# Kernel tuning notes

Hardware: AMD Instinct MI355X
Metric: run time of the kernel (lower is better)

Reference implementation:

```python
import jax, jax.numpy as jnp
import numpy as np

N = 14541   # num entities (FB15k-237)
R = 64      # num relations / edge types
E = 16384   # edges per relation
F = 128     # feature_dim
H = 128     # hidden_dim
O = 64      # out_dim
LH = O // 2 # lstm hidden per direction


def setup_inputs() -> dict:
    key = jax.random.key(0)
    ks = jax.random.split(key, 12)
    s = 0.05
    return {
        "node_ids": jnp.arange(N, dtype=jnp.int32),
        "src": jax.random.randint(ks[0], (R, E), 0, N, dtype=jnp.int32),
        "dst": jax.random.randint(ks[1], (R, E), 0, N, dtype=jnp.int32),
        "entity_emb": jax.random.normal(ks[2], (N, F), jnp.float32) * s,
        "W1": jax.random.normal(ks[3], (R, F, H), jnp.float32) * s,
        "b1": jax.random.normal(ks[4], (R, H), jnp.float32) * s,
        "W2": jax.random.normal(ks[5], (R, H, O), jnp.float32) * s,
        "b2": jax.random.normal(ks[6], (R, O), jnp.float32) * s,
        "w_ih": jax.random.normal(ks[7], (2, 4 * LH, O), jnp.float32) * s,
        "w_hh": jax.random.normal(ks[8], (2, 4 * LH, LH), jnp.float32) * s,
        "b_ih": jax.random.normal(ks[9], (2, 4 * LH), jnp.float32) * s,
        "b_hh": jax.random.normal(ks[10], (2, 4 * LH), jnp.float32) * s,
    }


def hetero_graph_conv(x, src, dst, W, b):
    """DGL HeteroGraphConv({rel: GraphConv(norm='both')}, aggregate='mean').
    x: [N, Fin]; src/dst: [R, E]; W: [R, Fin, Fout]; b: [R, Fout]."""
    n = x.shape[0]
    rid = jnp.arange(R, dtype=src.dtype)[:, None]
    fsrc = (rid * n + src).reshape(-1)            # per-(relation,node) flat ids
    fdst = (rid * n + dst).reshape(-1)
    ones = jnp.ones(fsrc.shape[0], x.dtype)
    deg_out = jax.ops.segment_sum(ones, fsrc, R * n)  # [R*N]
    deg_in = jax.ops.segment_sum(ones, fdst, R * n)
    norm_out = jnp.where(deg_out > 0, deg_out, 1.0) ** -0.5
    norm_in = jnp.where(deg_in > 0, deg_in, 1.0) ** -0.5
    # gather-normalize-scatter (sum) per relation, norm='both'
    msg = x[src.reshape(-1)] * norm_out[fsrc][:, None]     # [R*E, Fin]
    agg = jax.ops.segment_sum(msg, fdst, R * n)            # [R*N, Fin]
    agg = (agg * norm_in[:, None]).reshape(R, n, -1)
    out = jnp.einsum('rnf,rfo->rno', agg, W) + b[:, None, :]
    return out.mean(axis=0)  # mean aggregate across relations -> [N, Fout]


def lstm_one_step(x, w_ih, b_ih, b_hh):
    """Single-timestep LSTM direction with zero initial (h, c). PyTorch gate order i,f,g,o."""
    gates = x @ w_ih.T + b_ih + b_hh              # [N, 4*LH]
    i, f, g, o = jnp.split(gates, 4, axis=-1)
    c = jax.nn.sigmoid(i) * jnp.tanh(g)           # f*c0 = 0
    return jax.nn.sigmoid(o) * jnp.tanh(c)


def reference(node_ids, src, dst, entity_emb, W1, b1, W2, b2, w_ih, w_hh, b_ih, b_hh):
    x = entity_emb[node_ids]                                   # embedding lookup [N, F]
    h = jax.nn.relu(hetero_graph_conv(x, src, dst, W1, b1))    # conv1 + ReLU
    h = hetero_graph_conv(h, src, dst, W2, b2)                 # conv2 -> [N, O]
    # BiLSTM over seq_len=1 (unsqueeze(1) in torch): h0=c0=0 so W_hh contributes nothing
    h_fwd = lstm_one_step(h, w_ih[0], b_ih[0], b_hh[0])
    h_bwd = lstm_one_step(h, w_ih[1], b_ih[1], b_hh[1])
    return jnp.concatenate([h_fwd, h_bwd], axis=-1)            # [N, O]
```

## Files before the change

### kernel.cpp

```cpp
#include <hip/hip_runtime.h>

#define NN 14541
#define RR 64
#define EE 16384
#define EMAX (RR * EE)
#define RN (RR * NN)
#define NT 64
#define TILES 228
#define RGROUPS 8
#define RPG 8
#define NBPT 58
#define NWORDS (NBPT * 256 / 2)

typedef unsigned short u16;
typedef __attribute__((ext_vector_type(8))) short bf16x8;
typedef __attribute__((ext_vector_type(4))) float f32x4;

__device__ __forceinline__ u16 f2b(float f) {
  unsigned u = __builtin_bit_cast(unsigned, f);
  u += 0x7fffu + ((u >> 16) & 1u);
  return (u16)(u >> 16);
}
__device__ __forceinline__ float b2f(short h) {
  unsigned u = ((unsigned)(u16)h) << 16;
  return __builtin_bit_cast(float, u);
}
__device__ __forceinline__ unsigned cvtpk(float lo, float hi) {
  unsigned r;
  asm("v_cvt_pk_bf16_f32 %0, %1, %2" : "=v"(r) : "v"(lo), "v"(hi));
  return r;
}
__device__ __forceinline__ float sigm(float x) { return 1.0f / (1.0f + expf(-x)); }

__device__ __forceinline__ void gload_lds16(const void* g, void* l) {
  __builtin_amdgcn_global_load_lds(
      (const __attribute__((address_space(1))) unsigned int*)g,
      (__attribute__((address_space(3))) unsigned int*)l, 16, 0, 0);
}

__global__ __launch_bounds__(256) void build_k(
    const int* __restrict__ src, const int* __restrict__ dst,
    int* __restrict__ row_ptr, int* __restrict__ ssrc,
    float* __restrict__ scoef, float* __restrict__ tmpc,
    const float* __restrict__ W1, const float* __restrict__ W2,
    const float* __restrict__ b1, const float* __restrict__ b2,
    const float* __restrict__ emb,
    u16* __restrict__ W1T, u16* __restrict__ W2T,
    u16* __restrict__ emb_bf, float* __restrict__ mb1, float* __restrict__ mb2)
{
  __shared__ __align__(16) unsigned smem[NWORDS * 2];
  __shared__ int wsum[4];
  const int b = blockIdx.x, t = threadIdx.x;

  if (b < 64) {
    unsigned* cd = smem;
    unsigned* cs = smem + NWORDS;
    const int r = b;
    const int ebase = r * EE;

    for (int i = t; i < NWORDS; i += 256) { cd[i] = 0; cs[i] = 0; }
    __syncthreads();
    for (int e = t; e < EE; e += 256) {
      int d = dst[ebase + e], s = src[ebase + e];
      atomicAdd(&cd[d >> 1], (d & 1) ? 0x10000u : 1u);
      atomicAdd(&cs[s >> 1], (s & 1) ? 0x10000u : 1u);
    }
    __syncthreads();
    for (int e = t; e < EE; e += 256) {
      int d = dst[ebase + e], s = src[ebase + e];
      int cdd = (cd[d >> 1] >> ((d & 1) * 16)) & 0xffff;
      int css = (cs[s >> 1] >> ((s & 1) * 16)) & 0xffff;
      tmpc[ebase + e] = rsqrtf((float)cdd) * rsqrtf((float)css) * 0.015625f;
    }
    const int base = t * (NBPT / 2);
    int tot = 0;
    #pragma unroll
    for (int j = 0; j < NBPT / 2; j++) {
      unsigned w = cd[base + j];
      tot += (int)(w & 0xffff) + (int)(w >> 16);
    }
    const int lane = t & 63, wv = t >> 6;
    int x = tot;
    #pragma unroll
    for (int o = 1; o < 64; o <<= 1) { int y = __shfl_up(x, o, 64); if (lane >= o) x += y; }
    if (lane == 63) wsum[wv] = x;
    __syncthreads();
    int runl = x - tot;
    #pragma unroll
    for (int j = 0; j < 3; j++) if (j < wv) runl += wsum[j];
    const int nb0 = t * NBPT;
    #pragma unroll
    for (int j = 0; j < NBPT / 2; j++) {
      unsigned w = cd[base + j];
      int c0 = (int)(w & 0xffff), c1 = (int)(w >> 16);
      int n0 = nb0 + 2 * j;
      if (n0 <= NN)     row_ptr[r * NN + n0]     = r * EE + runl;
      if (n0 + 1 <= NN) row_ptr[r * NN + n0 + 1] = r * EE + runl + c0;
      cd[base + j] = (unsigned)(runl | ((runl + c0) << 16));
      runl += c0 + c1;
    }
    __syncthreads();
    for (int e = t; e < EE; e += 256) {
      int d = dst[ebase + e], s = src[ebase + e];
      unsigned old = atomicAdd(&cd[d >> 1], (d & 1) ? 0x10000u : 1u);
      int slot = ebase + (int)((old >> ((d & 1) * 16)) & 0xffff);
      ssrc[slot] = s;
      scoef[slot] = tmpc[ebase + e];
    }
    return;
  }

  float (*T)[65] = (float(*)[65])smem;
  const int bb = b - 64;
  if (bb < 128) {
    const int h = t & 63, kof = t >> 6;
    const int r = bb >> 1, hbase = (bb & 1) << 6;
    const float* Wr = W1 + (r << 14) + hbase;
    for (int k0 = 0; k0 < 128; k0 += 4) {
      int k = k0 + kof;
      T[k][h] = Wr[k * 128 + h];
    }
    __syncthreads();
    u16* dstp = W1T + (r << 14) + hbase * 128;
    #pragma unroll
    for (int it = 0; it < 4; ++it) {
      int p = it * 256 + t;
      int hh = p >> 4, v = p & 15;
      int hg = hbase + hh;
      bf16x8 o;
      #pragma unroll
      for (int j = 0; j < 8; j++)
        o[j] = (short)f2b(T[((v ^ (hg & 7)) << 3) + j][hh]);
      *(bf16x8*)(dstp + hh * 128 + v * 8) = o;
    }
  } else if (bb < 192) {
    const int h = t & 63, kof = t >> 6;
    const int r = bb - 128;
    const float* Wr = W2 + (r << 13);
    for (int k0 = 0; k0 < 128; k0 += 4) {
      int k = k0 + kof;
      T[k][h] = Wr[k * 64 + h];
    }
    __syncthreads();
    u16* dstp = W2T + (r << 13);
    #pragma unroll
    for (int it = 0; it < 4; ++it) {
      int p = it * 256 + t;
      int hh = p >> 4, v = p & 15;
      bf16x8 o;
      #pragma unroll
      for (int j = 0; j < 8; j++)
        o[j] = (short)f2b(T[((v ^ (hh & 7)) << 3) + j][hh]);
      *(bf16x8*)(dstp + hh * 128 + v * 8) = o;
    }
  } else if (bb < 2011) {
    int i = ((bb - 192) * 256 + t) * 4;
    if (i < NN * 128) {
      float4 vv = *(const float4*)(emb + i);
      ushort4 o;
      o.x = f2b(vv.x); o.y = f2b(vv.y); o.z = f2b(vv.z); o.w = f2b(vv.w);
      *(ushort4*)(emb_bf + i) = o;
    }
  } else {
    if (t < 128) { float s = 0.f; for (int r = 0; r < RR; r++) s += b1[r * 128 + t]; mb1[t] = s * (1.f/64.f); }
    if (t < 64)  { float s = 0.f; for (int r = 0; r < RR; r++) s += b2[r * 64 + t];  mb2[t] = s * (1.f/64.f); }
  }
}

__global__ __launch_bounds__(256, 2) void conv1_k(
    const u16* __restrict__ emb_bf, const int* __restrict__ row_ptr,
    const int* __restrict__ ssrc, const float* __restrict__ scoef,
    const u16* __restrict__ W1T, float* __restrict__ out1, int gstr)
{
  __shared__ __align__(16) u16 Bs[128 * 128];

  const int tid = threadIdx.x;
  const int g = blockIdx.x & 7, t = blockIdx.x >> 3;
  const int nb = t * NT;
  const int lane = tid & 63, wid = tid >> 6, c15 = lane & 15, kg = lane >> 4;
  const int rq = lane >> 2, q = lane & 3;
  const int nq = nb + wid * 16 + rq;
  const int srcl = c15 * 4 + kg;
  const int gbase = g * RPG;

  f32x4 acc[8];
  #pragma unroll
  for (int b = 0; b < 8; b++) acc[b] = (f32x4){0.f, 0.f, 0.f, 0.f};

  int rc0 = row_ptr[gbase * NN + nq];
  int rc1 = row_ptr[gbase * NN + nq + 1];
  int ps[4]; float pc[4];
  {
    const int d0 = rc1 - rc0;
    #pragma unroll
    for (int m = 0; m < 4; m++) {
      ps[m] = 0; pc[m] = 0.f;
      if (m < d0) { ps[m] = ssrc[rc0 + m]; pc[m] = scoef[rc0 + m]; }
    }
  }

  for (int rr = 0; rr < RPG; ++rr) {
    const int r = gbase + rr;
    {
      const u16* src_g = W1T + (r << 14);
      #pragma unroll
      for (int it = 0; it < 8; ++it)
        gload_lds16(src_g + (it * 256 + tid) * 8, (u16*)Bs + (it * 256 + wid * 64) * 8);
    }
    int nr0 = 0, nr1 = 0;
    if (rr + 1 < RPG) { nr0 = row_ptr[(r + 1) * NN + nq]; nr1 = row_ptr[(r + 1) * NN + nq + 1]; }
    const int d = rc1 - rc0;
    float a[4][8];
    #pragma unroll
    for (int w = 0; w < 4; w++)
      #pragma unroll
      for (int j = 0; j < 8; j++) a[w][j] = 0.f;
    #pragma unroll
    for (int m = 0; m < 4; m++) {
      if (m < d) {
        const bf16x8* xr = (const bf16x8*)(emb_bf + (size_t)ps[m] * 128);
        #pragma unroll
        for (int w = 0; w < 4; w++) {
          bf16x8 v = xr[w * 4 + q];
          #pragma unroll
          for (int j = 0; j < 8; j++) a[w][j] = fmaf(pc[m], b2f(v[j]), a[w][j]);
        }
      }
    }
    for (int p = 4; __any(p < d); ++p) {
      if (p < d) {
        int sx = ssrc[rc0 + p];
        float c = scoef[rc0 + p];
        const bf16x8* xr = (const bf16x8*)(emb_bf + (size_t)sx * 128);
        #pragma unroll
        for (int w = 0; w < 4; w++) {
          bf16x8 v = xr[w * 4 + q];
          #pragma unroll
          for (int j = 0; j < 8; j++) a[w][j] = fmaf(c, b2f(v[j]), a[w][j]);
        }
      }
    }
    int qs[4]; float qc[4];
    {
      const int ndg = nr1 - nr0;
      #pragma unroll
      for (int m = 0; m < 4; m++) {
        qs[m] = 0; qc[m] = 0.f;
        if (m < ndg) { qs[m] = ssrc[nr0 + m]; qc[m] = scoef[nr0 + m]; }
      }
    }
    bf16x8 af[4];
    #pragma unroll
    for (int kk = 0; kk < 4; kk++) {
      unsigned w0 = cvtpk(a[kk][0], a[kk][1]);
      unsigned w1 = cvtpk(a[kk][2], a[kk][3]);
      unsigned w2 = cvtpk(a[kk][4], a[kk][5]);
      unsigned w3 = cvtpk(a[kk][6], a[kk][7]);
      uint4 uu;
      uu.x = (unsigned)__shfl((int)w0, srcl);
      uu.y = (unsigned)__shfl((int)w1, srcl);
      uu.z = (unsigned)__shfl((int)w2, srcl);
      uu.w = (unsigned)__shfl((int)w3, srcl);
      af[kk] = __builtin_bit_cast(bf16x8, uu);
    }
    __syncthreads();
    #pragma unroll
    for (int tc = 0; tc < 8; tc++) {
      const int hh = tc * 16 + c15;
      #pragma unroll
      for (int kk = 0; kk < 4; kk++) {
        int u = kk * 4 + kg;
        bf16x8 bfr = *(const bf16x8*)(Bs + hh * 128 + ((u ^ (hh & 7)) << 3));
        acc[tc] = __builtin_amdgcn_mfma_f32_16x16x32_bf16(af[kk], bfr, acc[tc], 0, 0, 0);
      }
    }
    rc0 = nr0; rc1 = nr1;
    #pragma unroll
    for (int m = 0; m < 4; m++) { ps[m] = qs[m]; pc[m] = qc[m]; }
    if (rr + 1 < RPG) __syncthreads();
  }
  float* base = out1 + (size_t)g * gstr;
  #pragma unroll
  for (int qi = 0; qi < 4; qi++) {
    const int nn2 = nb + wid * 16 + kg * 4 + qi;
    if (nn2 < NN) {
      float* po = base + (size_t)nn2 * 128 + c15;
      if (gstr) {
        #pragma unroll
        for (int tc = 0; tc < 8; tc++) po[tc * 16] = acc[tc][qi];
      } else {
        #pragma unroll
        for (int tc = 0; tc < 8; tc++) atomicAdd(po + tc * 16, acc[tc][qi]);
      }
    }
  }
}

__global__ void relu_k(const float* __restrict__ out1, const float* __restrict__ mb1,
                       u16* __restrict__ h1, int gstr) {
  int i = (blockIdx.x * 256 + threadIdx.x) * 4;
  if (i >= NN * 128) return;
  f32x4 v = *(const f32x4*)(mb1 + (i & 127));
  if (gstr) {
    #pragma unroll
    for (int g = 0; g < RGROUPS; g++)
      v += __builtin_nontemporal_load((const f32x4*)(out1 + (size_t)g * gstr + i));
  } else {
    v += *(const f32x4*)(out1 + i);
  }
  ushort4 o;
  o.x = f2b(v.x > 0.f ? v.x : 0.f);
  o.y = f2b(v.y > 0.f ? v.y : 0.f);
  o.z = f2b(v.z > 0.f ? v.z : 0.f);
  o.w = f2b(v.w > 0.f ? v.w : 0.f);
  *(ushort4*)(h1 + i) = o;
}

__global__ __launch_bounds__(256, 2) void conv2_k(
    const u16* __restrict__ h1, const int* __restrict__ row_ptr,
    const int* __restrict__ ssrc, const float* __restrict__ scoef,
    const u16* __restrict__ W2T, float* __restrict__ out2, int gstr)
{
  __shared__ __align__(16) u16 Bs[2][64 * 128];

  const int tid = threadIdx.x;
  const int g = blockIdx.x & 7, t = blockIdx.x >> 3;
  const int nb = t * NT;
  const int lane = tid & 63, wid = tid >> 6, c15 = lane & 15, kg = lane >> 4;
  const int rq = lane >> 2, q = lane & 3;
  const int nq = nb + wid * 16 + rq;
  const int srcl = c15 * 4 + kg;
  const int gbase = g * RPG;

  f32x4 acc[4];
  #pragma unroll
  for (int b = 0; b < 4; b++) acc[b] = (f32x4){0.f, 0.f, 0.f, 0.f};

  int rc0 = row_ptr[gbase * NN + nq];
  int rc1 = row_ptr[gbase * NN + nq + 1];
  int ps[4]; float pc[4];
  {
    const int d0 = rc1 - rc0;
    #pragma unroll
    for (int m = 0; m < 4; m++) {
      ps[m] = 0; pc[m] = 0.f;
      if (m < d0) { ps[m] = ssrc[rc0 + m]; pc[m] = scoef[rc0 + m]; }
    }
  }
  {
    const u16* src_g = W2T + (gbase << 13);
    #pragma unroll
    for (int it = 0; it < 4; ++it)
      gload_lds16(src_g + (it * 256 + tid) * 8, (u16*)Bs[0] + (it * 256 + wid * 64) * 8);
  }

  for (int rr = 0; rr < RPG; ++rr) {
    const int r = gbase + rr;
    if (rr + 1 < RPG) {
      const u16* src_g = W2T + ((r + 1) << 13);
      #pragma unroll
      for (int it = 0; it < 4; ++it)
        gload_lds16(src_g + (it * 256 + tid) * 8, (u16*)Bs[(rr + 1) & 1] + (it * 256 + wid * 64) * 8);
    }
    int nr0 = 0, nr1 = 0;
    if (rr + 1 < RPG) { nr0 = row_ptr[(r + 1) * NN + nq]; nr1 = row_ptr[(r + 1) * NN + nq + 1]; }
    const int d = rc1 - rc0;
    float a[4][8];
    #pragma unroll
    for (int w = 0; w < 4; w++)
      #pragma unroll
      for (int j = 0; j < 8; j++) a[w][j] = 0.f;
    #pragma unroll
    for (int m = 0; m < 4; m++) {
      if (m < d) {
        const bf16x8* xr = (const bf16x8*)(h1 + (size_t)ps[m] * 128);
        #pragma unroll
        for (int w = 0; w < 4; w++) {
          bf16x8 v = xr[w * 4 + q];
          #pragma unroll
          for (int j = 0; j < 8; j++) a[w][j] = fmaf(pc[m], b2f(v[j]), a[w][j]);
        }
      }
    }
    for (int p = 4; __any(p < d); ++p) {
      if (p < d) {
        int sx = ssrc[rc0 + p];
        float c = scoef[rc0 + p];
        const bf16x8* xr = (const bf16x8*)(h1 + (size_t)sx * 128);
        #pragma unroll
        for (int w = 0; w < 4; w++) {
          bf16x8 v = xr[w * 4 + q];
          #pragma unroll
          for (int j = 0; j < 8; j++) a[w][j] = fmaf(c, b2f(v[j]), a[w][j]);
        }
      }
    }
    int qs[4]; float qc[4];
    {
      const int ndg = nr1 - nr0;
      #pragma unroll
      for (int m = 0; m < 4; m++) {
        qs[m] = 0; qc[m] = 0.f;
        if (m < ndg) { qs[m] = ssrc[nr0 + m]; qc[m] = scoef[nr0 + m]; }
      }
    }
    bf16x8 af[4];
    #pragma unroll
    for (int kk = 0; kk < 4; kk++) {
      unsigned w0 = cvtpk(a[kk][0], a[kk][1]);
      unsigned w1 = cvtpk(a[kk][2], a[kk][3]);
      unsigned w2 = cvtpk(a[kk][4], a[kk][5]);
      unsigned w3 = cvtpk(a[kk][6], a[kk][7]);
      uint4 uu;
      uu.x = (unsigned)__shfl((int)w0, srcl);
      uu.y = (unsigned)__shfl((int)w1, srcl);
      uu.z = (unsigned)__shfl((int)w2, srcl);
      uu.w = (unsigned)__shfl((int)w3, srcl);
      af[kk] = __builtin_bit_cast(bf16x8, uu);
    }
    __syncthreads();
    const u16* Bcur = Bs[rr & 1];
    #pragma unroll
    for (int tc = 0; tc < 4; tc++) {
      const int hh = tc * 16 + c15;
      #pragma unroll
      for (int kk = 0; kk < 4; kk++) {
        int u = kk * 4 + kg;
        bf16x8 bfr = *(const bf16x8*)(Bcur + hh * 128 + ((u ^ (hh & 7)) << 3));
        acc[tc] = __builtin_amdgcn_mfma_f32_16x16x32_bf16(af[kk], bfr, acc[tc], 0, 0, 0);
      }
    }
    rc0 = nr0; rc1 = nr1;
    #pragma unroll
    for (int m = 0; m < 4; m++) { ps[m] = qs[m]; pc[m] = qc[m]; }
  }
  float* base = out2 + (size_t)g * gstr;
  #pragma unroll
  for (int qi = 0; qi < 4; qi++) {
    const int nn2 = nb + wid * 16 + kg * 4 + qi;
    if (nn2 < NN) {
      float* po = base + (size_t)nn2 * 64 + c15;
      if (gstr) {
        #pragma unroll
        for (int tc = 0; tc < 4; tc++) po[tc * 16] = acc[tc][qi];
      } else {
        #pragma unroll
        for (int tc = 0; tc < 4; tc++) atomicAdd(po + tc * 16, acc[tc][qi]);
      }
    }
  }
}

__global__ __launch_bounds__(256) void lstm_k(const float* __restrict__ out2, const float* __restrict__ mb2,
                                              const float* __restrict__ w_ih, const float* __restrict__ b_ih,
                                              const float* __restrict__ b_hh, float* __restrict__ out,
                                              int gstr) {
  __shared__ float hs[16][64];
  const int tid = threadIdx.x, s = tid >> 6, k = tid & 63;
  const int nb = blockIdx.x * 16;
  #pragma unroll
  for (int j = 0; j < 4; j++) {
    int n = nb + s * 4 + j;
    if (n < NN) {
      float v = mb2[k];
      if (gstr) {
        #pragma unroll
        for (int g = 0; g < RGROUPS; g++)
          v += __builtin_nontemporal_load(out2 + (size_t)g * gstr + n * 64 + k);
      } else {
        v += out2[n * 64 + k];
      }
      hs[s * 4 + j][k] = v;
    }
  }
  __syncthreads();
  const int d = k >> 5, jj = k & 31;
  const float* wb = w_ih + d * 128 * 64;
  const float bi = b_ih[d * 128 + jj]      + b_hh[d * 128 + jj];
  const float bg = b_ih[d * 128 + 64 + jj] + b_hh[d * 128 + 64 + jj];
  const float bo = b_ih[d * 128 + 96 + jj] + b_hh[d * 128 + 96 + jj];
  const float* wi = wb + jj * 64;
  const float* wg = wb + (64 + jj) * 64;
  const float* wo = wb + (96 + jj) * 64;
  float gi[4] = {bi, bi, bi, bi}, gg[4] = {bg, bg, bg, bg}, go[4] = {bo, bo, bo, bo};
  #pragma unroll 8
  for (int kk = 0; kk < 64; kk++) {
    float w_i = wi[kk], w_g = wg[kk], w_o = wo[kk];
    #pragma unroll
    for (int j = 0; j < 4; j++) {
      float hv = hs[s * 4 + j][kk];
      gi[j] = fmaf(hv, w_i, gi[j]);
      gg[j] = fmaf(hv, w_g, gg[j]);
      go[j] = fmaf(hv, w_o, go[j]);
    }
  }
  #pragma unroll
  for (int j = 0; j < 4; j++) {
    int n = nb + s * 4 + j;
    if (n < NN) {
      float c = sigm(gi[j]) * tanhf(gg[j]);
      out[n * 64 + k] = sigm(go[j]) * tanhf(c);
    }
  }
}

extern "C" void kernel_launch(void* const* d_in, const int* in_sizes, int n_in,
                              void* d_out, int out_size, void* d_ws, size_t ws_size,
                              hipStream_t stream) {
  const int*   src  = (const int*)d_in[1];
  const int*   dst  = (const int*)d_in[2];
  const float* emb  = (const float*)d_in[3];
  const float* W1   = (const float*)d_in[4];
  const float* b1   = (const float*)d_in[5];
  const float* W2   = (const float*)d_in[6];
  const float* b2   = (const float*)d_in[7];
  const float* w_ih = (const float*)d_in[8];
  const float* b_ih = (const float*)d_in[10];
  const float* b_hh = (const float*)d_in[11];
  float* out = (float*)d_out;

  char* ws = (char*)d_ws;
  size_t off = 0;
  float* out1f  = (float*)(ws + off); off += (size_t)NN * 128 * 4;
  float* out2f  = (float*)(ws + off); off += (size_t)NN * 64 * 4;
  size_t zb_fb = off;
  int*   row_ptr= (int*)(ws + off);   off += (size_t)(RN + 256) * 4;
  int*   ssrc   = (int*)(ws + off);   off += (size_t)EMAX * 4;
  float* scoef  = (float*)(ws + off); off += (size_t)EMAX * 4;
  float* tmpc   = (float*)(ws + off); off += (size_t)EMAX * 4;
  u16*   emb_bf = (u16*)(ws + off);   off += (size_t)NN * 128 * 2;
  u16*   h1     = (u16*)(ws + off);   off += (size_t)NN * 128 * 2;
  u16*   W1T    = (u16*)(ws + off);   off += (size_t)RR * 128 * 128 * 2;
  u16*   W2T    = (u16*)(ws + off);   off += (size_t)RR * 64 * 128 * 2;
  float* mb1    = (float*)(ws + off); off += 512;
  float* mb2    = (float*)(ws + off); off += 256;
  float* out1g  = (float*)(ws + off); off += (size_t)RGROUPS * NN * 128 * 4;
  float* out2g  = (float*)(ws + off); off += (size_t)RGROUPS * NN * 64 * 4;

  const bool slices = ws_size >= off;
  float* o1 = slices ? out1g : out1f;
  float* o2 = slices ? out2g : out2f;
  const int gs1 = slices ? NN * 128 : 0;
  const int gs2 = slices ? NN * 64 : 0;

  if (!slices) hipMemsetAsync(d_ws, 0, zb_fb, stream);
  build_k<<<64 + 2012, 256, 0, stream>>>(src, dst, row_ptr, ssrc, scoef, tmpc,
                                         W1, W2, b1, b2, emb, W1T, W2T, emb_bf, mb1, mb2);
  conv1_k<<<TILES * RGROUPS, 256, 0, stream>>>(emb_bf, row_ptr, ssrc, scoef, W1T, o1, gs1);
  relu_k<<<(NN * 128 / 4 + 255) / 256, 256, 0, stream>>>(o1, mb1, h1, gs1);
  conv2_k<<<TILES * RGROUPS, 256, 0, stream>>>(h1, row_ptr, ssrc, scoef, W2T, o2, gs2);
  lstm_k<<<(NN + 15) / 16, 256, 0, stream>>>(o2, mb2, w_ih, b_ih, b_hh, out, gs2);
}
```

Baseline: 311.8 us.

## Fuse ReLU and LSTM epilogues into conv kernels via last-block counters

Removes the separate relu_k and lstm_k launches. Each conv kernel now bumps a per-tile atomic counter after writing its relation-group partial. The last of the 8 group blocks for that tile sums the slices and applies bias+ReLU (conv1) or the bias plus the LSTM gate math (conv2). This saves two launches and lets the reduction read partials that may still be in cache. In exchange it adds threadfence/atomic synchronisation and a serial tail done by only one block per tile, and the counters are reset in build_k.

After: 529.8 us. 69.9% more time.

```diff
diff --git a/kernel.cpp b/kernel.cpp
--- a/kernel.cpp
+++ b/kernel.cpp
@@ -46,7 +46,8 @@
     const float* __restrict__ b1, const float* __restrict__ b2,
     const float* __restrict__ emb,
     u16* __restrict__ W1T, u16* __restrict__ W2T,
-    u16* __restrict__ emb_bf, float* __restrict__ mb1, float* __restrict__ mb2)
+    u16* __restrict__ emb_bf, float* __restrict__ mb1, float* __restrict__ mb2,
+    int* __restrict__ cnt)
 {
   __shared__ __align__(16) unsigned smem[NWORDS * 2];
   __shared__ int wsum[4];
@@ -164,15 +165,18 @@
   } else {
     if (t < 128) { float s = 0.f; for (int r = 0; r < RR; r++) s += b1[r * 128 + t]; mb1[t] = s * (1.f/64.f); }
     if (t < 64)  { float s = 0.f; for (int r = 0; r < RR; r++) s += b2[r * 64 + t];  mb2[t] = s * (1.f/64.f); }
+    for (int i = t; i < 512; i += 256) cnt[i] = 0;
   }
 }
 
 __global__ __launch_bounds__(256, 2) void conv1_k(
     const u16* __restrict__ emb_bf, const int* __restrict__ row_ptr,
     const int* __restrict__ ssrc, const float* __restrict__ scoef,
-    const u16* __restrict__ W1T, float* __restrict__ out1, int gstr)
+    const u16* __restrict__ W1T, float* __restrict__ out1, int gstr,
+    const float* __restrict__ mb1, u16* __restrict__ h1, int* __restrict__ cnt1)
 {
   __shared__ __align__(16) u16 Bs[128 * 128];
+  __shared__ int lastf;
 
   const int tid = threadIdx.x;
   const int g = blockIdx.x & 7, t = blockIdx.x >> 3;
@@ -279,49 +283,68 @@
     for (int m = 0; m < 4; m++) { ps[m] = qs[m]; pc[m] = qc[m]; }
     if (rr + 1 < RPG) __syncthreads();
   }
-  float* base = out1 + (size_t)g * gstr;
-  #pragma unroll
-  for (int qi = 0; qi < 4; qi++) {
-    const int nn2 = nb + wid * 16 + kg * 4 + qi;
-    if (nn2 < NN) {
-      float* po = base + (size_t)nn2 * 128 + c15;
-      if (gstr) {
-        #pragma unroll
-        for (int tc = 0; tc < 8; tc++) po[tc * 16] = acc[tc][qi];
-      } else {
-        #pragma unroll
-        for (int tc = 0; tc < 8; tc++) atomicAdd(po + tc * 16, acc[tc][qi]);
-      }
-    }
-  }
-}
-
-__global__ void relu_k(const float* __restrict__ out1, const float* __restrict__ mb1,
-                       u16* __restrict__ h1, int gstr) {
-  int i = (blockIdx.x * 256 + threadIdx.x) * 4;
-  if (i >= NN * 128) return;
-  f32x4 v = *(const f32x4*)(mb1 + (i & 127));
-  if (gstr) {
-    #pragma unroll
-    for (int g = 0; g < RGROUPS; g++)
-      v += __builtin_nontemporal_load((const f32x4*)(out1 + (size_t)g * gstr + i));
-  } else {
-    v += *(const f32x4*)(out1 + i);
-  }
-  ushort4 o;
-  o.x = f2b(v.x > 0.f ? v.x : 0.f);
-  o.y = f2b(v.y > 0.f ? v.y : 0.f);
-  o.z = f2b(v.z > 0.f ? v.z : 0.f);
-  o.w = f2b(v.w > 0.f ? v.w : 0.f);
-  *(ushort4*)(h1 + i) = o;
+  {
+    float* base = out1 + (size_t)g * gstr;
+    #pragma unroll
+    for (int qi = 0; qi < 4; qi++) {
+      const int nn2 = nb + wid * 16 + kg * 4 + qi;
+      if (nn2 < NN) {
+        float* po = base + (size_t)nn2 * 128 + c15;
+        if (gstr) {
+          #pragma unroll
+          for (int tc = 0; tc < 8; tc++) po[tc * 16] = acc[tc][qi];
+        } else {
+          #pragma unroll
+          for (int tc = 0; tc < 8; tc++) atomicAdd(po + tc * 16, acc[tc][qi]);
+        }
+      }
+    }
+  }
+  __syncthreads();
+  if (tid == 0) {
+    __threadfence();
+    int old = atomicAdd(&cnt1[t], 1);
+    lastf = (old == RGROUPS - 1) ? 1 : 0;
+    if (lastf) __threadfence();
+  }
+  __syncthreads();
+  if (lastf) {
+    #pragma unroll
+    for (int it = 0; it < 8; ++it) {
+      int idx = it * 256 + tid;
+      int row = idx >> 5, col4 = (idx & 31) * 4;
+      int n = nb + row;
+      if (n < NN) {
+        size_t o = (size_t)n * 128 + col4;
+        f32x4 v = *(const f32x4*)(mb1 + col4);
+        if (gstr) {
+          #pragma unroll
+          for (int g2 = 0; g2 < RGROUPS; g2++)
+            v += *(const f32x4*)(out1 + (size_t)g2 * gstr + o);
+        } else {
+          v += *(const f32x4*)(out1 + o);
+        }
+        ushort4 ov;
+        ov.x = f2b(v.x > 0.f ? v.x : 0.f);
+        ov.y = f2b(v.y > 0.f ? v.y : 0.f);
+        ov.z = f2b(v.z > 0.f ? v.z : 0.f);
+        ov.w = f2b(v.w > 0.f ? v.w : 0.f);
+        *(ushort4*)(h1 + o) = ov;
+      }
+    }
+  }
 }
 
 __global__ __launch_bounds__(256, 2) void conv2_k(
     const u16* __restrict__ h1, const int* __restrict__ row_ptr,
     const int* __restrict__ ssrc, const float* __restrict__ scoef,
-    const u16* __restrict__ W2T, float* __restrict__ out2, int gstr)
+    const u16* __restrict__ W2T, float* __restrict__ out2, int gstr,
+    const float* __restrict__ mb2, const float* __restrict__ w_ih,
+    const float* __restrict__ b_ih, const float* __restrict__ b_hh,
+    float* __restrict__ outF, int* __restrict__ cnt2)
 {
   __shared__ __align__(16) u16 Bs[2][64 * 128];
+  __shared__ int lastf;
 
   const int tid = threadIdx.x;
   const int g = blockIdx.x & 7, t = blockIdx.x >> 3;
@@ -434,72 +457,82 @@
     #pragma unroll
     for (int m = 0; m < 4; m++) { ps[m] = qs[m]; pc[m] = qc[m]; }
   }
-  float* base = out2 + (size_t)g * gstr;
+  {
+    float* base = out2 + (size_t)g * gstr;
+    #pragma unroll
+    for (int qi = 0; qi < 4; qi++) {
+      const int nn2 = nb + wid * 16 + kg * 4 + qi;
+      if (nn2 < NN) {
+        float* po = base + (size_t)nn2 * 64 + c15;
+        if (gstr) {
+          #pragma unroll
+          for (int tc = 0; tc < 4; tc++) po[tc * 16] = acc[tc][qi];
+        } else {
+          #pragma unroll
+          for (int tc = 0; tc < 4; tc++) atomicAdd(po + tc * 16, acc[tc][qi]);
+        }
+      }
+    }
+  }
+  __syncthreads();
+  if (tid == 0) {
+    __threadfence();
+    int old = atomicAdd(&cnt2[t], 1);
+    lastf = (old == RGROUPS - 1) ? 1 : 0;
+    if (lastf) __threadfence();
+  }
+  __syncthreads();
+  if (!lastf) return;
+
+  float* hs = (float*)Bs;
   #pragma unroll
-  for (int qi = 0; qi < 4; qi++) {
-    const int nn2 = nb + wid * 16 + kg * 4 + qi;
-    if (nn2 < NN) {
-      float* po = base + (size_t)nn2 * 64 + c15;
+  for (int it = 0; it < 16; ++it) {
+    int idx = it * 256 + tid;
+    int row = idx >> 6, k = idx & 63;
+    int n = nb + row;
+    float v = mb2[k];
+    if (n < NN) {
       if (gstr) {
         #pragma unroll
-        for (int tc = 0; tc < 4; tc++) po[tc * 16] = acc[tc][qi];
+        for (int g2 = 0; g2 < RGROUPS; g2++)
+          v += out2[(size_t)g2 * gstr + (size_t)n * 64 + k];
       } else {
-        #pragma unroll
-        for (int tc = 0; tc < 4; tc++) atomicAdd(po + tc * 16, acc[tc][qi]);
-      }
-    }
-  }
-}
-
-__global__ __launch_bounds__(256) void lstm_k(const float* __restrict__ out2, const float* __restrict__ mb2,
-                                              const float* __restrict__ w_ih, const float* __restrict__ b_ih,
-                                              const float* __restrict__ b_hh, float* __restrict__ out,
-                                              int gstr) {
-  __shared__ float hs[16][64];
-  const int tid = threadIdx.x, s = tid >> 6, k = tid & 63;
-  const int nb = blockIdx.x * 16;
-  #pragma unroll
-  for (int j = 0; j < 4; j++) {
-    int n = nb + s * 4 + j;
-    if (n < NN) {
-      float v = mb2[k];
-      if (gstr) {
-        #pragma unroll
-        for (int g = 0; g < RGROUPS; g++)
-          v += __builtin_nontemporal_load(out2 + (size_t)g * gstr + n * 64 + k);
-      } else {
-        v += out2[n * 64 + k];
-      }
-      hs[s * 4 + j][k] = v;
-    }
+        v += out2[(size_t)n * 64 + k];
+      }
+    }
+    hs[row * 64 + k] = v;
   }
   __syncthreads();
-  const int d = k >> 5, jj = k & 31;
-  const float* wb = w_ih + d * 128 * 64;
-  const float bi = b_ih[d * 128 + jj]      + b_hh[d * 128 + jj];
-  const float bg = b_ih[d * 128 + 64 + jj] + b_hh[d * 128 + 64 + jj];
-  const float bo = b_ih[d * 128 + 96 + jj] + b_hh[d * 128 + 96 + jj];
+  const int k = tid & 63, sg = tid >> 6;
+  const int dd = k >> 5, jj = k & 31;
+  const float* wb = w_ih + dd * 128 * 64;
+  const float bi = b_ih[dd * 128 + jj]      + b_hh[dd * 128 + jj];
+  const float bg = b_ih[dd * 128 + 64 + jj] + b_hh[dd * 128 + 64 + jj];
+  const float bo = b_ih[dd * 128 + 96 + jj] + b_hh[dd * 128 + 96 + jj];
   const float* wi = wb + jj * 64;
   const float* wg = wb + (64 + jj) * 64;
   const float* wo = wb + (96 + jj) * 64;
-  float gi[4] = {bi, bi, bi, bi}, gg[4] = {bg, bg, bg, bg}, go[4] = {bo, bo, bo, bo};
-  #pragma unroll 8
+  float gi[16], gg[16], go[16];
+  #pragma unroll
+  for (int j = 0; j < 16; j++) { gi[j] = bi; gg[j] = bg; go[j] = bo; }
+  #pragma unroll 4
   for (int kk = 0; kk < 64; kk++) {
     float w_i = wi[kk], w_g = wg[kk], w_o = wo[kk];
-    #pragma unroll
-    for (int j = 0; j < 4; j++) {
-      float hv = hs[s * 4 + j][kk];
+    const float* hrow = hs + (sg * 16) * 64 + kk;
+    #pragma unroll
+    for (int j = 0; j < 16; j++) {
+      float hv = hrow[j * 64];
       gi[j] = fmaf(hv, w_i, gi[j]);
       gg[j] = fmaf(hv, w_g, gg[j]);
       go[j] = fmaf(hv, w_o, go[j]);
     }
   }
   #pragma unroll
-  for (int j = 0; j < 4; j++) {
-    int n = nb + s * 4 + j;
+  for (int j = 0; j < 16; j++) {
+    int n = nb + sg * 16 + j;
     if (n < NN) {
       float c = sigm(gi[j]) * tanhf(gg[j]);
-      out[n * 64 + k] = sigm(go[j]) * tanhf(c);
+      outF[(size_t)n * 64 + k] = sigm(go[j]) * tanhf(c);
     }
   }
 }
@@ -534,6 +567,7 @@
   u16*   W2T    = (u16*)(ws + off);   off += (size_t)RR * 64 * 128 * 2;
   float* mb1    = (float*)(ws + off); off += 512;
   float* mb2    = (float*)(ws + off); off += 256;
+  int*   cnt    = (int*)(ws + off);   off += 512 * 4;
   float* out1g  = (float*)(ws + off); off += (size_t)RGROUPS * NN * 128 * 4;
   float* out2g  = (float*)(ws + off); off += (size_t)RGROUPS * NN * 64 * 4;
 
@@ -545,9 +579,9 @@
 
   if (!slices) hipMemsetAsync(d_ws, 0, zb_fb, stream);
   build_k<<<64 + 2012, 256, 0, stream>>>(src, dst, row_ptr, ssrc, scoef, tmpc,
-                                         W1, W2, b1, b2, emb, W1T, W2T, emb_bf, mb1, mb2);
-  conv1_k<<<TILES * RGROUPS, 256, 0, stream>>>(emb_bf, row_ptr, ssrc, scoef, W1T, o1, gs1);
-  relu_k<<<(NN * 128 / 4 + 255) / 256, 256, 0, stream>>>(o1, mb1, h1, gs1);
-  conv2_k<<<TILES * RGROUPS, 256, 0, stream>>>(h1, row_ptr, ssrc, scoef, W2T, o2, gs2);
-  lstm_k<<<(NN + 15) / 16, 256, 0, stream>>>(o2, mb2, w_ih, b_ih, b_hh, out, gs2);
-}
+                                         W1, W2, b1, b2, emb, W1T, W2T, emb_bf, mb1, mb2, cnt);
+  conv1_k<<<TILES * RGROUPS, 256, 0, stream>>>(emb_bf, row_ptr, ssrc, scoef, W1T, o1, gs1,
+                                               mb1, h1, cnt);
+  conv2_k<<<TILES * RGROUPS, 256, 0, stream>>>(h1, row_ptr, ssrc, scoef, W2T, o2, gs2,
+                                               mb2, w_ih, b_ih, b_hh, out, cnt + 256);
+}
```
